# Kernel tuning notes

Measured on AMD Instinct MI355X. Metric: run time of the kernel, lower is better.

The kernel has to match this reference:

```python
import jax, jax.numpy as jnp
import numpy as np

N_BASIS = 8
CUTOFF = 5.0
NORM_FACTOR = 16.0


def setup_inputs() -> dict:
    key = jax.random.key(0)
    ks = jax.random.split(key, 10)
    N, E, C = 20000, 320000, 32
    s = 1.0 / np.sqrt(C)
    return {
        "node0": jax.random.normal(ks[0], (N, C), jnp.float32),
        "node1": jax.random.normal(ks[1], (N, C, 3), jnp.float32),
        "node2": jax.random.normal(ks[2], (N, C, 3, 3), jnp.float32),
        "rij": jax.random.normal(ks[3], (E, 3), jnp.float32) * 1.5,
        "Wrad": jax.random.normal(ks[4], (11, N_BASIS, C), jnp.float32) * 0.3,
        "U": jax.random.normal(ks[5], (3, C, C), jnp.float32) * s,
        "V": jax.random.normal(ks[6], (8, C, C), jnp.float32) * s,
        "Wg": jax.random.normal(ks[7], (3, C, C), jnp.float32) * s,
        "idx_i": jax.random.randint(ks[8], (E,), 0, N),
        "idx_j": jax.random.randint(ks[9], (E,), 0, N),
    }


def reference(node0, node1, node2, rij, Wrad, U, V, Wg, idx_i, idx_j):
    N, C = node0.shape
    # radial basis (Gaussian RBF * cosine cutoff envelope)
    dist = jnp.sqrt(jnp.sum(rij * rij, -1) + 1e-12)           # [E]
    rhat = rij / dist[:, None]                                 # [E,3]
    centers = jnp.linspace(0.5, CUTOFF, N_BASIS, dtype=node0.dtype)
    fc = 0.5 * (jnp.cos(jnp.pi * jnp.clip(dist / CUTOFF, 0.0, 1.0)) + 1.0)
    rbf = jnp.exp(-4.0 * (dist[:, None] - centers) ** 2) * fc[:, None]  # [E,B]
    # per-coupling-path radial filters: 11 paths (in_way, r_way, out_way)
    w = jnp.einsum('eb,pbc->pec', rbf, Wrad)                   # [11,E,C]
    # gather neighbor (node_j) features per edge
    g0 = node0[idx_j]                                          # [E,C]
    g1 = node1[idx_j]                                          # [E,C,3]
    g2 = node2[idx_j]                                          # [E,C,3,3]
    m1 = rhat                                                  # [E,3]
    m2 = rhat[:, :, None] * rhat[:, None, :]                   # [E,3,3]
    # graph conv: contract node_j tensor with r-way moment, weighted by radial filter
    # paths: 0:(0,0,0) 1:(0,1,1) 2:(0,2,2) 3:(1,0,1) 4:(1,1,0) 5:(1,1,2)
    #        6:(1,2,1) 7:(2,0,2) 8:(2,1,1) 9:(2,2,0) 10:(2,2,2)
    msg0 = (g0 * w[0]
            + jnp.einsum('eca,ea->ec', g1, m1) * w[4]
            + jnp.einsum('ecab,eab->ec', g2, m2) * w[9])
    msg1 = (jnp.einsum('ec,ea->eca', g0 * w[1], m1)
            + g1 * w[3][:, :, None]
            + jnp.einsum('eca,eab->ecb', g1, m2) * w[6][:, :, None]
            + jnp.einsum('ecab,eb->eca', g2, m1) * w[8][:, :, None])
    msg2 = (jnp.einsum('ec,eab->ecab', g0 * w[2], m2)
            + jnp.einsum('eca,eb->ecab', g1 * w[5][:, :, None], m1)
            + g2 * w[7][:, :, None, None]
            + jnp.einsum('ecab,ebd->ecad', g2, m2) * w[10][:, :, None, None])
    # scatter_add aggregation into per-atom features, normalized
    a0 = jax.ops.segment_sum(msg0, idx_i, num_segments=N) / NORM_FACTOR
    a1 = jax.ops.segment_sum(msg1, idx_i, num_segments=N) / NORM_FACTOR
    a2 = jax.ops.segment_sum(msg2, idx_i, num_segments=N) / NORM_FACTOR
    # multi-body self-interaction (2-body linear U + 3-body products V)
    y0 = (jnp.einsum('nc,cd->nd', a0, U[0])
          + jnp.einsum('nc,cd->nd', a0 * a0, V[0])
          + jnp.einsum('nc,cd->nd', jnp.einsum('nca,nca->nc', a1, a1), V[3])
          + jnp.einsum('nc,cd->nd', jnp.einsum('ncab,ncab->nc', a2, a2), V[6]))
    y1 = (jnp.einsum('nca,cd->nda', a1, U[1])
          + jnp.einsum('nca,cd->nda', a0[:, :, None] * a1, V[1])
          + jnp.einsum('nca,cd->nda', jnp.einsum('nca,ncab->ncb', a1, a2), V[5]))
    y2 = (jnp.einsum('ncab,cd->ndab', a2, U[2])
          + jnp.einsum('ncab,cd->ndab', a0[:, :, None, None] * a2, V[2])
          + jnp.einsum('ncab,cd->ndab', a1[:, :, :, None] * a1[:, :, None, :], V[4])
          + jnp.einsum('ncab,cd->ndab', jnp.einsum('ncab,ncbd->ncad', a2, a2), V[7]))
    # gated nonlinearity (scalar channel gates tensor ways) + residual add
    new0 = node0 + jax.nn.silu(y0 @ Wg[0])
    new1 = node1 + y1 * jax.nn.silu(y0 @ Wg[1])[:, :, None]
    new2 = node2 + y2 * jax.nn.silu(y0 @ Wg[2])[:, :, None, None]
    return (new0, new1, new2)
```

## Files before the change

### kernel.cpp

```cpp
#include <hip/hip_runtime.h>
#include <hip/hip_fp16.h>

#define NCH 32
#define NB 8
#define NPB 8

typedef __attribute__((ext_vector_type(2))) _Float16 half2r;

__device__ __forceinline__ unsigned short f2h(float f) {
    return __half_as_ushort(__float2half_rn(f));
}
__device__ __forceinline__ float h2f_lo(unsigned int u) {
    half2r v = __builtin_bit_cast(half2r, u);
    return (float)v.x;
}
__device__ __forceinline__ float h2f_hi(unsigned int u) {
    half2r v = __builtin_bit_cast(half2r, u);
    return (float)v.y;
}
__device__ __forceinline__ unsigned int pack2h(float lo, float hi) {
    return (unsigned int)f2h(lo) | ((unsigned int)f2h(hi) << 16);
}

__device__ __forceinline__ float fdot2u(unsigned int a, unsigned int b, float c) {
#if __has_builtin(__builtin_amdgcn_fdot2)
    return __builtin_amdgcn_fdot2(__builtin_bit_cast(half2r, a),
                                  __builtin_bit_cast(half2r, b), c, false);
#else
    half2r av = __builtin_bit_cast(half2r, a);
    half2r bv = __builtin_bit_cast(half2r, b);
    return c + (float)av.x * (float)bv.x + (float)av.y * (float)bv.y;
#endif
}

__device__ __forceinline__ void acc8h(float& y, uint4 w, uint4 f) {
    y = fdot2u(w.x, f.x, y);
    y = fdot2u(w.y, f.y, y);
    y = fdot2u(w.z, f.z, y);
    y = fdot2u(w.w, f.w, y);
}
__device__ __forceinline__ void acc8fh(float& y, uint4 w, float4 a, float4 b) {
    y += h2f_lo(w.x) * a.x + h2f_hi(w.x) * a.y + h2f_lo(w.y) * a.z + h2f_hi(w.y) * a.w
       + h2f_lo(w.z) * b.x + h2f_hi(w.z) * b.y + h2f_lo(w.w) * b.z + h2f_hi(w.w) * b.w;
}

__global__ __launch_bounds__(256) void prep_kernel(
    const float* __restrict__ node0, const float* __restrict__ node1,
    const float* __restrict__ node2,
    const float* __restrict__ U, const float* __restrict__ V,
    const float* __restrict__ Wg, const float* __restrict__ Wrad,
    uint2* __restrict__ t0g, uint4* __restrict__ t1g,
    unsigned short* __restrict__ t2g,
    unsigned short* __restrict__ wswz, unsigned int* __restrict__ wradp,
    int N, int TB)
{
    __shared__ float s1[8 * 96];
    __shared__ float s2[8 * 288];
    const int bx = blockIdx.x;

    if (bx < TB) {
        const int nb0 = bx * 8;
        const int remN = N - nb0;
        if (remN >= 8) {
            const float4* src1 = reinterpret_cast<const float4*>(node1 + (size_t)nb0 * 96);
            float4* d1 = reinterpret_cast<float4*>(s1);
            for (int i = threadIdx.x; i < 192; i += 256) d1[i] = src1[i];
            const float4* src2 = reinterpret_cast<const float4*>(node2 + (size_t)nb0 * 288);
            float4* d2 = reinterpret_cast<float4*>(s2);
            for (int i = threadIdx.x; i < 576; i += 256) d2[i] = src2[i];
        } else {
            const int tot1 = remN * 96;
            for (int i = threadIdx.x; i < 768; i += 256)
                s1[i] = (i < tot1) ? node1[(size_t)nb0 * 96 + i] : 0.f;
            const int tot2 = remN * 288;
            for (int i = threadIdx.x; i < 2304; i += 256)
                s2[i] = (i < tot2) ? node2[(size_t)nb0 * 288 + i] : 0.f;
        }
        __syncthreads();

        const int g = threadIdx.x >> 5;
        const int c = threadIdx.x & 31;
        const int n = nb0 + g;
        if (n >= N) return;

        float G0 = node0[(size_t)n * 32 + c];
        float G1[3];
        #pragma unroll
        for (int a = 0; a < 3; ++a) G1[a] = s1[g * 96 + c * 3 + a];
        float G2[9];
        #pragma unroll
        for (int k = 0; k < 9; ++k) G2[k] = s2[g * 288 + c * 9 + k];

        const size_t b = ((size_t)n << 5) + c;
        uint2 P0;
        P0.x = pack2h(G0, G1[0]);
        P0.y = pack2h(G1[1], G1[2]);
        uint4 P1;
        P1.x = pack2h(G2[0], G2[1]);
        P1.y = pack2h(G2[2], G2[3]);
        P1.z = pack2h(G2[4], G2[5]);
        P1.w = pack2h(G2[6], G2[7]);
        t0g[b] = P0;
        t1g[b] = P1;
        t2g[b] = f2h(G2[8]);
        return;
    }

    const int r = bx - TB;
    if (r < 56) {
        int idx = r * 256 + threadIdx.x;
        if (idx >= 14 * 1024) return;
        int m = idx >> 10, rr = idx & 1023;
        int c = rr >> 5, d = rr & 31;
        float v;
        if (m < 3)       v = U[m * 1024 + c * 32 + d];
        else if (m < 11) v = V[(m - 3) * 1024 + c * 32 + d];
        else             v = Wg[(m - 11) * 1024 + c * 32 + d];
        wswz[m * 1024 + (c >> 3) * 256 + d * 8 + (c & 7)] = f2h(v);
        return;
    }

    {
        int idx = (r - 56) * 256 + threadIdx.x;
        if (idx >= 11 * 4 * 32) return;
        int c = idx & 31, bb = (idx >> 5) & 3, p = idx >> 7;
        float lo = Wrad[p * 256 + (2 * bb) * 32 + c] * (1.0f / 16.0f);
        float hi = Wrad[p * 256 + (2 * bb + 1) * 32 + c] * (1.0f / 16.0f);
        wradp[c * 44 + p * 4 + bb] = pack2h(lo, hi);
    }
}

__global__ __launch_bounds__(256) void hist_kernel(
    const int* __restrict__ idx_i, int* __restrict__ counts, int E)
{
    int e = blockIdx.x * 256 + threadIdx.x;
    if (e < E) atomicAdd(&counts[idx_i[e]], 1);
}

__global__ __launch_bounds__(256) void scan_reduce_kernel(
    const int* __restrict__ counts, int* __restrict__ blocksums, int N)
{
    const int tid = threadIdx.x;
    const int base = blockIdx.x * 1024;
    int v = 0;
    #pragma unroll
    for (int k = 0; k < 4; ++k) {
        int i = base + tid * 4 + k;
        if (i < N) v += counts[i];
    }
    #pragma unroll
    for (int off = 1; off < 64; off <<= 1) v += __shfl_xor(v, off, 64);
    __shared__ int wsum[4];
    if ((tid & 63) == 0) wsum[tid >> 6] = v;
    __syncthreads();
    if (tid == 0) blocksums[blockIdx.x] = wsum[0] + wsum[1] + wsum[2] + wsum[3];
}

__global__ void scan_top_kernel(
    const int* __restrict__ blocksums, int* __restrict__ bases,
    int* __restrict__ offsets, int nb, int N)
{
    int l = threadIdx.x;
    int v = (l < nb) ? blocksums[l] : 0;
    int incl = v;
    #pragma unroll
    for (int off = 1; off < 64; off <<= 1) {
        int t = __shfl_up(incl, off, 64);
        if (l >= off) incl += t;
    }
    if (l < nb) bases[l] = incl - v;
    if (l == nb - 1) offsets[N] = incl;
}

__global__ __launch_bounds__(256) void scan_write_kernel(
    int* __restrict__ cursor, const int* __restrict__ bases,
    int* __restrict__ offsets, int N)
{
    const int tid = threadIdx.x;
    const int i0 = blockIdx.x * 1024 + tid * 4;
    int v[4]; int lsum = 0;
    #pragma unroll
    for (int k = 0; k < 4; ++k) {
        int i = i0 + k;
        v[k] = (i < N) ? cursor[i] : 0;
        lsum += v[k];
    }
    int incl = lsum;
    #pragma unroll
    for (int off = 1; off < 64; off <<= 1) {
        int t = __shfl_up(incl, off, 64);
        if ((tid & 63) >= off) incl += t;
    }
    __shared__ int wsum[4];
    if ((tid & 63) == 63) wsum[tid >> 6] = incl;
    __syncthreads();
    int add = bases[blockIdx.x];
    for (int w = 0; w < (tid >> 6); ++w) add += wsum[w];
    int run = add + incl - lsum;
    #pragma unroll
    for (int k = 0; k < 4; ++k) {
        int i = i0 + k;
        if (i < N) { offsets[i] = run; cursor[i] = run; run += v[k]; }
    }
}

__global__ __launch_bounds__(256) void scatter_meta_kernel(
    const int* __restrict__ idx_i, const int* __restrict__ idx_j,
    const float* __restrict__ rij, int* __restrict__ cursor,
    int* __restrict__ jord, float4* __restrict__ meta2, int E)
{
    int e = blockIdx.x * 256 + threadIdx.x;
    if (e >= E) return;
    float rx = rij[3 * e + 0], ry = rij[3 * e + 1], rz = rij[3 * e + 2];
    float sq = rx * rx + ry * ry + rz * rz + 1e-12f;
    float inv = rsqrtf(sq);
    float dist = sq * inv;
    float tcl = fminf(dist * 0.2f, 1.0f);
    float fc = 0.5f * (__cosf(3.14159265358979f * tcl) + 1.0f);
    float rbf[NB];
    #pragma unroll
    for (int b = 0; b < NB; ++b) {
        float dd = dist - (0.5f + (float)b * (4.5f / 7.0f));
        rbf[b] = __expf(-4.0f * dd * dd) * fc;
    }
    unsigned int rb01 = pack2h(rbf[0], rbf[1]);
    unsigned int rb23 = pack2h(rbf[2], rbf[3]);
    unsigned int rb45 = pack2h(rbf[4], rbf[5]);
    unsigned int rb67 = pack2h(rbf[6], rbf[7]);
    int slot = atomicAdd(&cursor[idx_i[e]], 1);
    jord[slot] = idx_j[e];
    meta2[2 * slot + 0] = make_float4(rx * inv, ry * inv, rz * inv, __uint_as_float(rb01));
    meta2[2 * slot + 1] = make_float4(__uint_as_float(rb23), __uint_as_float(rb45),
                                      __uint_as_float(rb67), 0.0f);
}

__device__ __forceinline__ void edge_compute(
    uint2 P0, uint4 P1, unsigned short g28, float4 M0, float4 M1,
    const uint4 wrq[11], float& A0, float (&A1)[3], float (&A2)[9])
{
    const float h0 = M0.x, h1 = M0.y, h2 = M0.z;
    const unsigned int rb01 = __float_as_uint(M0.w);
    const unsigned int rb23 = __float_as_uint(M1.x);
    const unsigned int rb45 = __float_as_uint(M1.y);
    const unsigned int rb67 = __float_as_uint(M1.z);

    float w[11];
    #pragma unroll
    for (int p = 0; p < 11; ++p)
        w[p] = fdot2u(rb01, wrq[p].x,
               fdot2u(rb23, wrq[p].y,
               fdot2u(rb45, wrq[p].z,
               fdot2u(rb67, wrq[p].w, 0.0f))));

    const float G0 = h2f_lo(P0.x);
    float G1[3];
    G1[0] = h2f_hi(P0.x); G1[1] = h2f_lo(P0.y); G1[2] = h2f_hi(P0.y);
    float G2[9];
    G2[0] = h2f_lo(P1.x); G2[1] = h2f_hi(P1.x);
    G2[2] = h2f_lo(P1.y); G2[3] = h2f_hi(P1.y);
    G2[4] = h2f_lo(P1.z); G2[5] = h2f_hi(P1.z);
    G2[6] = h2f_lo(P1.w); G2[7] = h2f_hi(P1.w);
    G2[8] = __half2float(__ushort_as_half(g28));

    const float hh[3] = {h0, h1, h2};
    const float s1 = G1[0] * h0 + G1[1] * h1 + G1[2] * h2;
    float tt[3];
    #pragma unroll
    for (int a = 0; a < 3; ++a)
        tt[a] = G2[a * 3 + 0] * h0 + G2[a * 3 + 1] * h1 + G2[a * 3 + 2] * h2;
    const float s2 = tt[0] * h0 + tt[1] * h1 + tt[2] * h2;

    A0 += G0 * w[0] + s1 * w[4] + s2 * w[9];
    #pragma unroll
    for (int a = 0; a < 3; ++a)
        A1[a] += (G0 * w[1] + s1 * w[6]) * hh[a] + G1[a] * w[3] + tt[a] * w[8];
    #pragma unroll
    for (int a = 0; a < 3; ++a) {
        float pre = G0 * w[2] * hh[a] + G1[a] * w[5] + tt[a] * w[10];
        #pragma unroll
        for (int b = 0; b < 3; ++b)
            A2[a * 3 + b] += pre * hh[b] + G2[a * 3 + b] * w[7];
    }
}

__global__ __launch_bounds__(256) void aggregate_kernel(
    const uint2* __restrict__ t0g, const uint4* __restrict__ t1g,
    const unsigned short* __restrict__ t2g, const unsigned int* __restrict__ wradp,
    const int* __restrict__ jord, const float4* __restrict__ meta2,
    const int* __restrict__ offsets,
    float* __restrict__ a0, float* __restrict__ a1, float* __restrict__ a2,
    int N)
{
    const int lane = threadIdx.x & 63;
    const int c = lane & 31;
    const int side = lane >> 5;
    const int n = blockIdx.x * 4 + (threadIdx.x >> 6);
    if (n >= N) return;

    uint4 wrq[11];
    {
        const uint4* wrv = reinterpret_cast<const uint4*>(wradp) + c * 11;
        #pragma unroll
        for (int p = 0; p < 11; ++p) wrq[p] = wrv[p];
    }

    const int beg = offsets[n], end = offsets[n + 1];
    const int deg = end - beg;

    float A0 = 0.f;
    float A1[3] = {0.f, 0.f, 0.f};
    float A2[9] = {0.f, 0.f, 0.f, 0.f, 0.f, 0.f, 0.f, 0.f, 0.f};

    if (deg > 0) {
        const int last = end - 1;
        int eA = beg + side;
        int eB = eA + 2;
        int jA2 = jord[min(eA + 4, last)];
        int jB2 = jord[min(eB + 4, last)];

        uint2 P0A, P0B; uint4 P1A, P1B; unsigned short s2A, s2B;
        float4 M0A, M1A, M0B, M1B;
        {
            const int jA = jord[min(eA, last)];
            const size_t b = ((size_t)jA << 5) + c;
            P0A = t0g[b]; P1A = t1g[b]; s2A = t2g[b];
            const int em = min(eA, last);
            M0A = meta2[2 * em]; M1A = meta2[2 * em + 1];
        }
        {
            const int jB = jord[min(eB, last)];
            const size_t b = ((size_t)jB << 5) + c;
            P0B = t0g[b]; P1B = t1g[b]; s2B = t2g[b];
            const int em = min(eB, last);
            M0B = meta2[2 * em]; M1B = meta2[2 * em + 1];
        }

        const int M = (deg + 3) >> 2;

#define SLOT_STEP(P0s, P1s, s2s, M0s, M1s, eS, jS2)                         \
        {                                                                   \
            const uint2 P0 = P0s; const uint4 P1 = P1s;                     \
            const unsigned short g28 = s2s;                                 \
            const float4 Mm0 = M0s, Mm1 = M1s;                              \
            const bool v = (eS < end);                                      \
            const int eSn = eS + 4;                                         \
            {                                                               \
                const size_t b = ((size_t)jS2 << 5) + c;                    \
                P0s = t0g[b]; P1s = t1g[b]; s2s = t2g[b];                   \
                const int em = min(eSn, last);                              \
                M0s = meta2[2 * em]; M1s = meta2[2 * em + 1];               \
            }                                                               \
            jS2 = jord[min(eSn + 4, last)];                                 \
            if (v) edge_compute(P0, P1, g28, Mm0, Mm1, wrq, A0, A1, A2);    \
            eS = eSn;                                                       \
        }

        for (int m = 0; m < M; ++m) {
            SLOT_STEP(P0A, P1A, s2A, M0A, M1A, eA, jA2)
            SLOT_STEP(P0B, P1B, s2B, M0B, M1B, eB, jB2)
        }
#undef SLOT_STEP
    }

    A0 += __shfl_xor(A0, 32, 64);
    #pragma unroll
    for (int a = 0; a < 3; ++a) A1[a] += __shfl_xor(A1[a], 32, 64);
    #pragma unroll
    for (int k = 0; k < 9; ++k) A2[k] += __shfl_xor(A2[k], 32, 64);

    if (side == 0) {
        a0[n * 32 + c] = A0;
        #pragma unroll
        for (int a = 0; a < 3; ++a) a1[n * 96 + a * 32 + c] = A1[a];
        #pragma unroll
        for (int k = 0; k < 9; ++k) a2[n * 288 + k * 32 + c] = A2[k];
    }
}

__global__ __launch_bounds__(256) void node_kernel(
    const float* __restrict__ node0, const float* __restrict__ node1,
    const float* __restrict__ node2, const unsigned short* __restrict__ wswz,
    float* __restrict__ out0, float* __restrict__ out1, float* __restrict__ out2,
    int N)
{
    __shared__ alignas(16) unsigned short wT[14 * 1024];
    __shared__ alignas(16) unsigned short feat[NPB * 49 * 32];
    __shared__ alignas(16) float y0s[NPB][32];

    {
        const uint4* src = reinterpret_cast<const uint4*>(wswz);
        uint4* dst = reinterpret_cast<uint4*>(wT);
        for (int i = threadIdx.x; i < 14 * 128; i += 256) dst[i] = src[i];
    }

    const int g = threadIdx.x >> 5;
    const int lane = threadIdx.x & 31;
    const int n = blockIdx.x * NPB + g;
    const bool active = (n < N);

    if (active) {
        const int c = lane;
        float A0 = out0[n * 32 + c];
        float A1[3], A2[9];
        #pragma unroll
        for (int a = 0; a < 3; ++a) A1[a] = out1[n * 96 + a * 32 + c];
        #pragma unroll
        for (int k = 0; k < 9; ++k) A2[k] = out2[n * 288 + k * 32 + c];

        unsigned short* F = &feat[g * 49 * 32];
        F[0 * 32 + c] = f2h(A0);
        F[1 * 32 + c] = f2h(A0 * A0);
        F[2 * 32 + c] = f2h(A1[0] * A1[0] + A1[1] * A1[1] + A1[2] * A1[2]);
        float n2 = 0.f;
        #pragma unroll
        for (int k = 0; k < 9; ++k) n2 += A2[k] * A2[k];
        F[3 * 32 + c] = f2h(n2);
        #pragma unroll
        for (int a = 0; a < 3; ++a) {
            F[(4 + a) * 32 + c] = f2h(A1[a]);
            F[(7 + a) * 32 + c] = f2h(A0 * A1[a]);
        }
        #pragma unroll
        for (int b = 0; b < 3; ++b) {
            float s = A1[0] * A2[0 * 3 + b] + A1[1] * A2[1 * 3 + b] + A1[2] * A2[2 * 3 + b];
            F[(10 + b) * 32 + c] = f2h(s);
        }
        #pragma unroll
        for (int k = 0; k < 9; ++k) {
            F[(13 + k) * 32 + c] = f2h(A2[k]);
            F[(22 + k) * 32 + c] = f2h(A0 * A2[k]);
        }
        #pragma unroll
        for (int a = 0; a < 3; ++a)
            #pragma unroll
            for (int b = 0; b < 3; ++b)
                F[(31 + a * 3 + b) * 32 + c] = f2h(A1[a] * A1[b]);
        #pragma unroll
        for (int a = 0; a < 3; ++a)
            #pragma unroll
            for (int dd = 0; dd < 3; ++dd) {
                float s = A2[a * 3 + 0] * A2[0 * 3 + dd] + A2[a * 3 + 1] * A2[1 * 3 + dd]
                        + A2[a * 3 + 2] * A2[2 * 3 + dd];
                F[(40 + a * 3 + dd) * 32 + c] = f2h(s);
            }
    }
    __syncthreads();

    const int d = lane;
    float y0v = 0.f;
    float y1v[3] = {0.f, 0.f, 0.f};
    float y2v[9] = {0.f, 0.f, 0.f, 0.f, 0.f, 0.f, 0.f, 0.f, 0.f};

    if (active) {
        const uint4* W4 = reinterpret_cast<const uint4*>(wT);
        const uint4* F4 = reinterpret_cast<const uint4*>(&feat[g * 49 * 32]);
        for (int q = 0; q < 4; ++q) {
            const int q32d = q * 32 + d;
            acc8h(y0v, W4[0 * 128 + q32d], F4[0 * 4 + q]);
            acc8h(y0v, W4[3 * 128 + q32d], F4[1 * 4 + q]);
            acc8h(y0v, W4[6 * 128 + q32d], F4[2 * 4 + q]);
            acc8h(y0v, W4[9 * 128 + q32d], F4[3 * 4 + q]);
            uint4 wU1 = W4[1 * 128 + q32d];
            uint4 wV1 = W4[4 * 128 + q32d];
            uint4 wV5 = W4[8 * 128 + q32d];
            #pragma unroll
            for (int a = 0; a < 3; ++a) {
                acc8h(y1v[a], wU1, F4[(4 + a) * 4 + q]);
                acc8h(y1v[a], wV1, F4[(7 + a) * 4 + q]);
                acc8h(y1v[a], wV5, F4[(10 + a) * 4 + q]);
            }
            uint4 wU2 = W4[2 * 128 + q32d];
            uint4 wV2 = W4[5 * 128 + q32d];
            uint4 wV4 = W4[7 * 128 + q32d];
            uint4 wV7 = W4[10 * 128 + q32d];
            #pragma unroll
            for (int k = 0; k < 9; ++k) {
                acc8h(y2v[k], wU2, F4[(13 + k) * 4 + q]);
                acc8h(y2v[k], wV2, F4[(22 + k) * 4 + q]);
                acc8h(y2v[k], wV4, F4[(31 + k) * 4 + q]);
                acc8h(y2v[k], wV7, F4[(40 + k) * 4 + q]);
            }
        }
        y0s[g][d] = y0v;
    }
    __syncthreads();

    if (!active) return;

    float t0 = 0.f, t1 = 0.f, t2 = 0.f;
    {
        const uint4* W4 = reinterpret_cast<const uint4*>(wT);
        const float4* Y4 = reinterpret_cast<const float4*>(y0s[g]);
        #pragma unroll
        for (int q = 0; q < 4; ++q) {
            const int q32d = q * 32 + d;
            float4 ya = Y4[2 * q], yb = Y4[2 * q + 1];
            acc8fh(t0, W4[11 * 128 + q32d], ya, yb);
            acc8fh(t1, W4[12 * 128 + q32d], ya, yb);
            acc8fh(t2, W4[13 * 128 + q32d], ya, yb);
        }
    }
    float s0 = t0 / (1.0f + __expf(-t0));
    float s1 = t1 / (1.0f + __expf(-t1));
    float s2 = t2 / (1.0f + __expf(-t2));

    out0[n * 32 + d] = node0[n * 32 + d] + s0;
    #pragma unroll
    for (int a = 0; a < 3; ++a)
        out1[n * 96 + d * 3 + a] = node1[n * 96 + d * 3 + a] + y1v[a] * s1;
    #pragma unroll
    for (int k = 0; k < 9; ++k)
        out2[n * 288 + d * 9 + k] = node2[n * 288 + d * 9 + k] + y2v[k] * s2;
}

extern "C" void kernel_launch(void* const* d_in, const int* in_sizes, int n_in,
                              void* d_out, int out_size, void* d_ws, size_t ws_size,
                              hipStream_t stream)
{
    const float* node0 = (const float*)d_in[0];
    const float* node1 = (const float*)d_in[1];
    const float* node2 = (const float*)d_in[2];
    const float* rij   = (const float*)d_in[3];
    const float* Wrad  = (const float*)d_in[4];
    const float* U     = (const float*)d_in[5];
    const float* V     = (const float*)d_in[6];
    const float* Wg    = (const float*)d_in[7];
    const int* idx_i   = (const int*)d_in[8];
    const int* idx_j   = (const int*)d_in[9];

    const int N = in_sizes[0] / 32;
    const int E = in_sizes[3] / 3;

    float* out0 = (float*)d_out;
    float* out1 = out0 + (size_t)N * 32;
    float* out2 = out1 + (size_t)N * 96;

    size_t off = 0;
    auto walloc = [&](size_t bytes) -> void* {
        off = (off + 63) & ~(size_t)63;
        void* p = (char*)d_ws + off;
        off += bytes;
        return p;
    };
    int*    cursor    = (int*)   walloc((size_t)N * 4);
    int*    offsets   = (int*)   walloc((size_t)(N + 1) * 4);
    int*    blocksums = (int*)   walloc(64 * 4);
    int*    bases     = (int*)   walloc(64 * 4);
    int*    jord      = (int*)   walloc((size_t)E * 4);
    float4* meta2     = (float4*)walloc((size_t)E * 2 * sizeof(float4));
    uint2*  t0g       = (uint2*) walloc((size_t)N * 32 * sizeof(uint2));
    uint4*  t1g       = (uint4*) walloc((size_t)N * 32 * sizeof(uint4));
    unsigned short* t2g = (unsigned short*)walloc((size_t)N * 32 * 2);
    unsigned short* wswz = (unsigned short*)walloc(14 * 1024 * 2);
    unsigned int*  wradp = (unsigned int*)walloc(11 * 4 * 32 * 4);
    (void)ws_size;

    const int nb = (N + 1023) / 1024;
    const int TB = (N + 7) / 8;

    hipMemsetAsync(cursor, 0, (size_t)N * sizeof(int), stream);

    prep_kernel<<<dim3(TB + 56 + 6), dim3(256), 0, stream>>>(
        node0, node1, node2, U, V, Wg, Wrad, t0g, t1g, t2g, wswz, wradp, N, TB);
    hist_kernel<<<dim3((E + 255) / 256), dim3(256), 0, stream>>>(idx_i, cursor, E);
    scan_reduce_kernel<<<dim3(nb), dim3(256), 0, stream>>>(cursor, blocksums, N);
    scan_top_kernel<<<dim3(1), dim3(64), 0, stream>>>(blocksums, bases, offsets, nb, N);
    scan_write_kernel<<<dim3(nb), dim3(256), 0, stream>>>(cursor, bases, offsets, N);
    scatter_meta_kernel<<<dim3((E + 255) / 256), dim3(256), 0, stream>>>(
        idx_i, idx_j, rij, cursor, jord, meta2, E);

    aggregate_kernel<<<dim3((N + 3) / 4), dim3(256), 0, stream>>>(
        t0g, t1g, t2g, wradp, jord, meta2, offsets, out0, out1, out2, N);

    node_kernel<<<dim3((N + NPB - 1) / NPB), dim3(256), 0, stream>>>(
        node0, node1, node2, wswz, out0, out1, out2, N);
}
```

Measured before the change: 262.2 us.

## Merge histogram into prep, single-block scan, and aggregate four nodes per wave

The edge-count histogram moves into prep_kernel, and the three-kernel scan becomes one 1024-thread scan kernel, which cuts launch count. The aggregate kernel now gives each wave four consecutive nodes. It walks their combined edge range with padded jord/meta arrays instead of min clamps, and routes each message to one of four register accumulators using a node tag stored in the meta padding. Radial weights are staged in LDS with a padded stride instead of held per lane in registers. The risks are more register pressure from the 4x13 accumulators, a branchy accumulate select, and the scan depending on N fitting within 1024*32 entries.

```diff
diff --git a/kernel.cpp b/kernel.cpp
--- a/kernel.cpp
+++ b/kernel.cpp
@@ -4,6 +4,8 @@
 #define NCH 32
 #define NB 8
 #define NPB 8
+#define EPAD 16
+#define WRS 52
 
 typedef __attribute__((ext_vector_type(2))) _Float16 half2r;
 
@@ -49,10 +51,11 @@
     const float* __restrict__ node2,
     const float* __restrict__ U, const float* __restrict__ V,
     const float* __restrict__ Wg, const float* __restrict__ Wrad,
+    const int* __restrict__ idx_i, int* __restrict__ cursor,
     uint2* __restrict__ t0g, uint4* __restrict__ t1g,
     unsigned short* __restrict__ t2g,
     unsigned short* __restrict__ wswz, unsigned int* __restrict__ wradp,
-    int N, int TB)
+    int N, int E, int TB)
 {
     __shared__ float s1[8 * 96];
     __shared__ float s2[8 * 288];
@@ -119,89 +122,74 @@
         wswz[m * 1024 + (c >> 3) * 256 + d * 8 + (c & 7)] = f2h(v);
         return;
     }
-
-    {
+    if (r < 62) {
         int idx = (r - 56) * 256 + threadIdx.x;
         if (idx >= 11 * 4 * 32) return;
         int c = idx & 31, bb = (idx >> 5) & 3, p = idx >> 7;
         float lo = Wrad[p * 256 + (2 * bb) * 32 + c] * (1.0f / 16.0f);
         float hi = Wrad[p * 256 + (2 * bb + 1) * 32 + c] * (1.0f / 16.0f);
-        wradp[c * 44 + p * 4 + bb] = pack2h(lo, hi);
-    }
-}
-
-__global__ __launch_bounds__(256) void hist_kernel(
-    const int* __restrict__ idx_i, int* __restrict__ counts, int E)
-{
-    int e = blockIdx.x * 256 + threadIdx.x;
-    if (e < E) atomicAdd(&counts[idx_i[e]], 1);
-}
-
-__global__ __launch_bounds__(256) void scan_reduce_kernel(
-    const int* __restrict__ counts, int* __restrict__ blocksums, int N)
+        wradp[c * WRS + p * 4 + bb] = pack2h(lo, hi);
+        return;
+    }
+    {
+        int e = (r - 62) * 256 + threadIdx.x;
+        if (e < E) atomicAdd(&cursor[idx_i[e]], 1);
+    }
+}
+
+#define KPT 32
+__global__ __launch_bounds__(1024) void scan_kernel(
+    int* __restrict__ cursor, int* __restrict__ offsets,
+    int* __restrict__ jord, int N, int E)
 {
     const int tid = threadIdx.x;
-    const int base = blockIdx.x * 1024;
-    int v = 0;
-    #pragma unroll
-    for (int k = 0; k < 4; ++k) {
-        int i = base + tid * 4 + k;
-        if (i < N) v += counts[i];
-    }
-    #pragma unroll
-    for (int off = 1; off < 64; off <<= 1) v += __shfl_xor(v, off, 64);
-    __shared__ int wsum[4];
-    if ((tid & 63) == 0) wsum[tid >> 6] = v;
-    __syncthreads();
-    if (tid == 0) blocksums[blockIdx.x] = wsum[0] + wsum[1] + wsum[2] + wsum[3];
-}
-
-__global__ void scan_top_kernel(
-    const int* __restrict__ blocksums, int* __restrict__ bases,
-    int* __restrict__ offsets, int nb, int N)
-{
-    int l = threadIdx.x;
-    int v = (l < nb) ? blocksums[l] : 0;
-    int incl = v;
+    const int lane = tid & 63;
+    const int wid = tid >> 6;
+    const int kpt = (N + 1023) >> 10;
+    const int base = tid * kpt;
+
+    int v[KPT];
+    int s = 0;
+    #pragma unroll
+    for (int k = 0; k < KPT; ++k) {
+        int i = base + k;
+        int x = 0;
+        if (k < kpt && i < N) x = cursor[i];
+        v[k] = x;
+        s += x;
+    }
+    int incl = s;
     #pragma unroll
     for (int off = 1; off < 64; off <<= 1) {
         int t = __shfl_up(incl, off, 64);
-        if (l >= off) incl += t;
-    }
-    if (l < nb) bases[l] = incl - v;
-    if (l == nb - 1) offsets[N] = incl;
-}
-
-__global__ __launch_bounds__(256) void scan_write_kernel(
-    int* __restrict__ cursor, const int* __restrict__ bases,
-    int* __restrict__ offsets, int N)
-{
-    const int tid = threadIdx.x;
-    const int i0 = blockIdx.x * 1024 + tid * 4;
-    int v[4]; int lsum = 0;
-    #pragma unroll
-    for (int k = 0; k < 4; ++k) {
-        int i = i0 + k;
-        v[k] = (i < N) ? cursor[i] : 0;
-        lsum += v[k];
-    }
-    int incl = lsum;
-    #pragma unroll
-    for (int off = 1; off < 64; off <<= 1) {
-        int t = __shfl_up(incl, off, 64);
-        if ((tid & 63) >= off) incl += t;
-    }
-    __shared__ int wsum[4];
-    if ((tid & 63) == 63) wsum[tid >> 6] = incl;
+        if (lane >= off) incl += t;
+    }
+    __shared__ int wsum[16];
+    if (lane == 63) wsum[wid] = incl;
     __syncthreads();
-    int add = bases[blockIdx.x];
-    for (int w = 0; w < (tid >> 6); ++w) add += wsum[w];
-    int run = add + incl - lsum;
-    #pragma unroll
-    for (int k = 0; k < 4; ++k) {
-        int i = i0 + k;
-        if (i < N) { offsets[i] = run; cursor[i] = run; run += v[k]; }
-    }
+    if (tid < 16) {
+        int x = wsum[tid];
+        #pragma unroll
+        for (int off = 1; off < 16; off <<= 1) {
+            int t = __shfl_up(x, off, 64);
+            if (tid >= off) x += t;
+        }
+        wsum[tid] = x;
+    }
+    __syncthreads();
+    int add = (wid > 0) ? wsum[wid - 1] : 0;
+    int run = add + incl - s;
+    #pragma unroll
+    for (int k = 0; k < KPT; ++k) {
+        int i = base + k;
+        if (k < kpt && i < N) {
+            offsets[i] = run;
+            cursor[i] = run;
+            run += v[k];
+        }
+    }
+    if (tid == 0) offsets[N] = wsum[15];
+    if (tid < EPAD) jord[E + tid] = 0;
 }
 
 __global__ __launch_bounds__(256) void scatter_meta_kernel(
@@ -223,20 +211,22 @@
         float dd = dist - (0.5f + (float)b * (4.5f / 7.0f));
         rbf[b] = __expf(-4.0f * dd * dd) * fc;
     }
-    unsigned int rb01 = pack2h(rbf[0], rbf[1]);
-    unsigned int rb23 = pack2h(rbf[2], rbf[3]);
-    unsigned int rb45 = pack2h(rbf[4], rbf[5]);
-    unsigned int rb67 = pack2h(rbf[6], rbf[7]);
-    int slot = atomicAdd(&cursor[idx_i[e]], 1);
+    const int i = idx_i[e];
+    int slot = atomicAdd(&cursor[i], 1);
     jord[slot] = idx_j[e];
-    meta2[2 * slot + 0] = make_float4(rx * inv, ry * inv, rz * inv, __uint_as_float(rb01));
-    meta2[2 * slot + 1] = make_float4(__uint_as_float(rb23), __uint_as_float(rb45),
-                                      __uint_as_float(rb67), 0.0f);
-}
-
-__device__ __forceinline__ void edge_compute(
+    meta2[2 * slot + 0] = make_float4(rx * inv, ry * inv, rz * inv,
+                                      __uint_as_float(pack2h(rbf[0], rbf[1])));
+    meta2[2 * slot + 1] = make_float4(__uint_as_float(pack2h(rbf[2], rbf[3])),
+                                      __uint_as_float(pack2h(rbf[4], rbf[5])),
+                                      __uint_as_float(pack2h(rbf[6], rbf[7])),
+                                      __uint_as_float((unsigned int)(i & 3)));
+}
+
+struct Msg { float m0; float m1[3]; float m2[9]; };
+
+__device__ __forceinline__ Msg msg_compute(
     uint2 P0, uint4 P1, unsigned short g28, float4 M0, float4 M1,
-    const uint4 wrq[11], float& A0, float (&A1)[3], float (&A2)[9])
+    const uint4* __restrict__ wr4)
 {
     const float h0 = M0.x, h1 = M0.y, h2 = M0.z;
     const unsigned int rb01 = __float_as_uint(M0.w);
@@ -246,11 +236,13 @@
 
     float w[11];
     #pragma unroll
-    for (int p = 0; p < 11; ++p)
-        w[p] = fdot2u(rb01, wrq[p].x,
-               fdot2u(rb23, wrq[p].y,
-               fdot2u(rb45, wrq[p].z,
-               fdot2u(rb67, wrq[p].w, 0.0f))));
+    for (int p = 0; p < 11; ++p) {
+        const uint4 q = wr4[p];
+        w[p] = fdot2u(rb01, q.x,
+               fdot2u(rb23, q.y,
+               fdot2u(rb45, q.z,
+               fdot2u(rb67, q.w, 0.0f))));
+    }
 
     const float G0 = h2f_lo(P0.x);
     float G1[3];
@@ -270,20 +262,24 @@
         tt[a] = G2[a * 3 + 0] * h0 + G2[a * 3 + 1] * h1 + G2[a * 3 + 2] * h2;
     const float s2 = tt[0] * h0 + tt[1] * h1 + tt[2] * h2;
 
-    A0 += G0 * w[0] + s1 * w[4] + s2 * w[9];
+    Msg r;
+    r.m0 = fmaf(s2, w[9], fmaf(s1, w[4], G0 * w[0]));
+    const float t01 = fmaf(s1, w[6], G0 * w[1]);
     #pragma unroll
     for (int a = 0; a < 3; ++a)
-        A1[a] += (G0 * w[1] + s1 * w[6]) * hh[a] + G1[a] * w[3] + tt[a] * w[8];
+        r.m1[a] = fmaf(tt[a], w[8], fmaf(G1[a], w[3], t01 * hh[a]));
+    const float g0w2 = G0 * w[2];
     #pragma unroll
     for (int a = 0; a < 3; ++a) {
-        float pre = G0 * w[2] * hh[a] + G1[a] * w[5] + tt[a] * w[10];
+        const float pre = fmaf(tt[a], w[10], fmaf(G1[a], w[5], g0w2 * hh[a]));
         #pragma unroll
         for (int b = 0; b < 3; ++b)
-            A2[a * 3 + b] += pre * hh[b] + G2[a * 3 + b] * w[7];
-    }
-}
-
-__global__ __launch_bounds__(256) void aggregate_kernel(
+            r.m2[a * 3 + b] = fmaf(G2[a * 3 + b], w[7], pre * hh[b]);
+    }
+    return r;
+}
+
+__global__ __launch_bounds__(256, 3) void aggregate_kernel(
     const uint2* __restrict__ t0g, const uint4* __restrict__ t1g,
     const unsigned short* __restrict__ t2g, const unsigned int* __restrict__ wradp,
     const int* __restrict__ jord, const float4* __restrict__ meta2,
@@ -291,51 +287,57 @@
     float* __restrict__ a0, float* __restrict__ a1, float* __restrict__ a2,
     int N)
 {
+    __shared__ unsigned int lwr[32 * WRS];
+    for (int i = threadIdx.x; i < 32 * WRS; i += 256) lwr[i] = wradp[i];
+    __syncthreads();
+
     const int lane = threadIdx.x & 63;
     const int c = lane & 31;
     const int side = lane >> 5;
-    const int n = blockIdx.x * 4 + (threadIdx.x >> 6);
-    if (n >= N) return;
-
-    uint4 wrq[11];
-    {
-        const uint4* wrv = reinterpret_cast<const uint4*>(wradp) + c * 11;
-        #pragma unroll
-        for (int p = 0; p < 11; ++p) wrq[p] = wrv[p];
-    }
-
-    const int beg = offsets[n], end = offsets[n + 1];
-    const int deg = end - beg;
-
-    float A0 = 0.f;
-    float A1[3] = {0.f, 0.f, 0.f};
-    float A2[9] = {0.f, 0.f, 0.f, 0.f, 0.f, 0.f, 0.f, 0.f, 0.f};
-
-    if (deg > 0) {
-        const int last = end - 1;
+    const int wv = blockIdx.x * 4 + (threadIdx.x >> 6);
+    const int n0 = wv * 4;
+    if (n0 >= N) return;
+
+    const uint4* wr4 = reinterpret_cast<const uint4*>(&lwr[c * WRS]);
+
+    const int beg = offsets[n0];
+    const int end = offsets[min(n0 + 4, N)];
+
+    float B0[4] = {0.f, 0.f, 0.f, 0.f};
+    float B1[4][3] = {};
+    float B2[4][9] = {};
+
+    if (end > beg) {
         int eA = beg + side;
         int eB = eA + 2;
-        int jA2 = jord[min(eA + 4, last)];
-        int jB2 = jord[min(eB + 4, last)];
+        int jA2 = jord[eA + 4];
+        int jB2 = jord[eB + 4];
 
         uint2 P0A, P0B; uint4 P1A, P1B; unsigned short s2A, s2B;
         float4 M0A, M1A, M0B, M1B;
         {
-            const int jA = jord[min(eA, last)];
-            const size_t b = ((size_t)jA << 5) + c;
+            const int j = jord[eA];
+            const size_t b = ((size_t)j << 5) + c;
             P0A = t0g[b]; P1A = t1g[b]; s2A = t2g[b];
-            const int em = min(eA, last);
-            M0A = meta2[2 * em]; M1A = meta2[2 * em + 1];
+            M0A = meta2[2 * eA]; M1A = meta2[2 * eA + 1];
         }
         {
-            const int jB = jord[min(eB, last)];
-            const size_t b = ((size_t)jB << 5) + c;
+            const int j = jord[eB];
+            const size_t b = ((size_t)j << 5) + c;
             P0B = t0g[b]; P1B = t1g[b]; s2B = t2g[b];
-            const int em = min(eB, last);
-            M0B = meta2[2 * em]; M1B = meta2[2 * em + 1];
-        }
-
-        const int M = (deg + 3) >> 2;
+            M0B = meta2[2 * eB]; M1B = meta2[2 * eB + 1];
+        }
+
+        const int M = (end - beg + 3) >> 2;
+
+#define ACCK(K)                                                             \
+        {                                                                   \
+            B0[K] += m.m0;                                                  \
+            B1[K][0] += m.m1[0]; B1[K][1] += m.m1[1]; B1[K][2] += m.m1[2];  \
+            B2[K][0] += m.m2[0]; B2[K][1] += m.m2[1]; B2[K][2] += m.m2[2];  \
+            B2[K][3] += m.m2[3]; B2[K][4] += m.m2[4]; B2[K][5] += m.m2[5];  \
+            B2[K][6] += m.m2[6]; B2[K][7] += m.m2[7]; B2[K][8] += m.m2[8];  \
+        }
 
 #define SLOT_STEP(P0s, P1s, s2s, M0s, M1s, eS, jS2)                         \
         {                                                                   \
@@ -347,33 +349,44 @@
             {                                                               \
                 const size_t b = ((size_t)jS2 << 5) + c;                    \
                 P0s = t0g[b]; P1s = t1g[b]; s2s = t2g[b];                   \
-                const int em = min(eSn, last);                              \
-                M0s = meta2[2 * em]; M1s = meta2[2 * em + 1];               \
+                M0s = meta2[2 * eSn]; M1s = meta2[2 * eSn + 1];             \
             }                                                               \
-            jS2 = jord[min(eSn + 4, last)];                                 \
-            if (v) edge_compute(P0, P1, g28, Mm0, Mm1, wrq, A0, A1, A2);    \
+            jS2 = jord[eSn + 4];                                            \
+            if (v) {                                                        \
+                const Msg m = msg_compute(P0, P1, g28, Mm0, Mm1, wr4);      \
+                const int nloc = ((int)__float_as_uint(Mm1.w)) & 3;         \
+                if (nloc == 0)      ACCK(0)                                 \
+                else if (nloc == 1) ACCK(1)                                 \
+                else if (nloc == 2) ACCK(2)                                 \
+                else                ACCK(3)                                 \
+            }                                                               \
             eS = eSn;                                                       \
         }
 
-        for (int m = 0; m < M; ++m) {
+        for (int m_ = 0; m_ < M; ++m_) {
             SLOT_STEP(P0A, P1A, s2A, M0A, M1A, eA, jA2)
             SLOT_STEP(P0B, P1B, s2B, M0B, M1B, eB, jB2)
         }
 #undef SLOT_STEP
-    }
-
-    A0 += __shfl_xor(A0, 32, 64);
-    #pragma unroll
-    for (int a = 0; a < 3; ++a) A1[a] += __shfl_xor(A1[a], 32, 64);
-    #pragma unroll
-    for (int k = 0; k < 9; ++k) A2[k] += __shfl_xor(A2[k], 32, 64);
-
-    if (side == 0) {
-        a0[n * 32 + c] = A0;
-        #pragma unroll
-        for (int a = 0; a < 3; ++a) a1[n * 96 + a * 32 + c] = A1[a];
-        #pragma unroll
-        for (int k = 0; k < 9; ++k) a2[n * 288 + k * 32 + c] = A2[k];
+#undef ACCK
+    }
+
+    #pragma unroll
+    for (int k = 0; k < 4; ++k) {
+        const int n = n0 + k;
+        float v0 = B0[k] + __shfl_xor(B0[k], 32, 64);
+        float v1[3], v2[9];
+        #pragma unroll
+        for (int a = 0; a < 3; ++a) v1[a] = B1[k][a] + __shfl_xor(B1[k][a], 32, 64);
+        #pragma unroll
+        for (int q = 0; q < 9; ++q) v2[q] = B2[k][q] + __shfl_xor(B2[k][q], 32, 64);
+        if (n < N && side == 0) {
+            a0[n * 32 + c] = v0;
+            #pragma unroll
+            for (int a = 0; a < 3; ++a) a1[n * 96 + a * 32 + c] = v1[a];
+            #pragma unroll
+            for (int q = 0; q < 9; ++q) a2[n * 288 + q * 32 + c] = v2[q];
+        }
     }
 }
 
@@ -544,32 +557,28 @@
     };
     int*    cursor    = (int*)   walloc((size_t)N * 4);
     int*    offsets   = (int*)   walloc((size_t)(N + 1) * 4);
-    int*    blocksums = (int*)   walloc(64 * 4);
-    int*    bases     = (int*)   walloc(64 * 4);
-    int*    jord      = (int*)   walloc((size_t)E * 4);
-    float4* meta2     = (float4*)walloc((size_t)E * 2 * sizeof(float4));
+    int*    jord      = (int*)   walloc((size_t)(E + EPAD) * 4);
+    float4* meta2     = (float4*)walloc((size_t)(E + EPAD) * 2 * sizeof(float4));
     uint2*  t0g       = (uint2*) walloc((size_t)N * 32 * sizeof(uint2));
     uint4*  t1g       = (uint4*) walloc((size_t)N * 32 * sizeof(uint4));
     unsigned short* t2g = (unsigned short*)walloc((size_t)N * 32 * 2);
     unsigned short* wswz = (unsigned short*)walloc(14 * 1024 * 2);
-    unsigned int*  wradp = (unsigned int*)walloc(11 * 4 * 32 * 4);
+    unsigned int*  wradp = (unsigned int*)walloc(32 * WRS * 4);
     (void)ws_size;
 
-    const int nb = (N + 1023) / 1024;
     const int TB = (N + 7) / 8;
+    const int HB = (E + 255) / 256;
 
     hipMemsetAsync(cursor, 0, (size_t)N * sizeof(int), stream);
 
-    prep_kernel<<<dim3(TB + 56 + 6), dim3(256), 0, stream>>>(
-        node0, node1, node2, U, V, Wg, Wrad, t0g, t1g, t2g, wswz, wradp, N, TB);
-    hist_kernel<<<dim3((E + 255) / 256), dim3(256), 0, stream>>>(idx_i, cursor, E);
-    scan_reduce_kernel<<<dim3(nb), dim3(256), 0, stream>>>(cursor, blocksums, N);
-    scan_top_kernel<<<dim3(1), dim3(64), 0, stream>>>(blocksums, bases, offsets, nb, N);
-    scan_write_kernel<<<dim3(nb), dim3(256), 0, stream>>>(cursor, bases, offsets, N);
+    prep_kernel<<<dim3(TB + 62 + HB), dim3(256), 0, stream>>>(
+        node0, node1, node2, U, V, Wg, Wrad, idx_i, cursor,
+        t0g, t1g, t2g, wswz, wradp, N, E, TB);
+    scan_kernel<<<dim3(1), dim3(1024), 0, stream>>>(cursor, offsets, jord, N, E);
     scatter_meta_kernel<<<dim3((E + 255) / 256), dim3(256), 0, stream>>>(
         idx_i, idx_j, rij, cursor, jord, meta2, E);
 
-    aggregate_kernel<<<dim3((N + 3) / 4), dim3(256), 0, stream>>>(
+    aggregate_kernel<<<dim3((N + 15) / 16), dim3(256), 0, stream>>>(
         t0g, t1g, t2g, wradp, jord, meta2, offsets, out0, out1, out2, N);
 
     node_kernel<<<dim3((N + NPB - 1) / NPB), dim3(256), 0, stream>>>(
```

Result: slower. 278.9 us (+6.4%).
